# Optimization experiments

Measured on AMD Instinct MI355X. Metric: run time of the kernel, lower is better.

## Reference

```python
import jax, jax.numpy as jnp
import numpy as np

DIM = 1024
NUM_HEADS = 16
HEAD_DIM = DIM // NUM_HEADS
SCALE = HEAD_DIM ** -0.5


def setup_inputs() -> dict:
    key = jax.random.key(0)
    ks = jax.random.split(key, 7)
    b, n = 2, 2048
    x = jax.random.normal(ks[0], (b, n, DIM), dtype=jnp.float32)
    s = DIM ** -0.5
    Wq = jax.random.normal(ks[1], (DIM, DIM), dtype=jnp.float32) * s
    bq = jax.random.normal(ks[2], (DIM,), dtype=jnp.float32) * 0.01
    Wk = jax.random.normal(ks[3], (DIM, DIM), dtype=jnp.float32) * s
    bk = jax.random.normal(ks[4], (DIM,), dtype=jnp.float32) * 0.01
    Wv = jax.random.normal(ks[5], (DIM, DIM), dtype=jnp.float32) * s
    bv = jax.random.normal(ks[6], (DIM,), dtype=jnp.float32) * 0.01
    return {"x": x, "Wq": Wq, "bq": bq, "Wk": Wk, "bk": bk, "Wv": Wv, "bv": bv}


def reference(x, Wq, bq, Wk, bk, Wv, bv):
    b, n, _ = x.shape
    # Linear projections (torch Linear: x @ W.T + b; here W stored as [in, out])
    q = x @ Wq + bq
    k = x @ Wk + bk
    v = x @ Wv + bv
    # split heads: [b, n, h*d] -> [b, h, n, d]
    split = lambda t: t.reshape(b, n, NUM_HEADS, HEAD_DIM).transpose(0, 2, 1, 3)
    q, k, v = split(q), split(k), split(v)
    sim = jnp.einsum('bhid,bhjd->bhij', q, k) * SCALE
    attn = jax.nn.softmax(sim, axis=-1)
    out = jnp.einsum('bhij,bhjd->bhid', attn, v)
    return out.transpose(0, 2, 1, 3).reshape(b, n, DIM)
```

## Files before the change

### kernel.cpp

```cpp
#include <hip/hip_runtime.h>
#include <cstdint>
#include <cstddef>

#define NB    2
#define SEQ   2048
#define DIMC  1024
#define NH    16
#define HDIM  64
#define MROWS (NB*SEQ)
#define NFEAT (3*DIMC)
#define KVBLK 64
#define NT    (SEQ/KVBLK)

typedef _Float16 half8 __attribute__((ext_vector_type(8)));
typedef _Float16 half4 __attribute__((ext_vector_type(4)));
typedef _Float16 half2v __attribute__((ext_vector_type(2)));
typedef __fp16   fp16x2 __attribute__((ext_vector_type(2)));
typedef float    f32x4 __attribute__((ext_vector_type(4)));

typedef const __attribute__((address_space(1))) void* gas_ptr;
typedef __attribute__((address_space(3))) void*       las_ptr;

__device__ __forceinline__ void gload_lds16(const void* g, void* l) {
    __builtin_amdgcn_global_load_lds((gas_ptr)g, (las_ptr)l, 16, 0, 0);
}

__device__ __forceinline__ int swz4(int r) { return (r ^ (r >> 2)) & 3; }

__device__ __forceinline__ float fast_exp2(float x) {
    float r;
    asm("v_exp_f32 %0, %1" : "=v"(r) : "v"(x));
    return r;
}

__device__ __forceinline__ half2v pk_f16(float a, float b) {
    fp16x2 r = __builtin_amdgcn_cvt_pkrtz(a, b);
    return __builtin_bit_cast(half2v, r);
}

__global__ __launch_bounds__(256) void k_convert_x(const float* __restrict__ x,
                                                   _Float16* __restrict__ x16) {
    int i = (blockIdx.x * 256 + threadIdx.x) * 4;
    float4 v = *reinterpret_cast<const float4*>(x + i);
    half4 h = { (_Float16)v.x, (_Float16)v.y, (_Float16)v.z, (_Float16)v.w };
    *reinterpret_cast<half4*>(x16 + i) = h;
}

__global__ __launch_bounds__(256) void k_transpose_w(const float* __restrict__ Wq,
                                                     const float* __restrict__ Wk,
                                                     const float* __restrict__ Wv,
                                                     _Float16* __restrict__ wt) {
    __shared__ float tile[64][65];
    const int bid  = blockIdx.x;
    const int midx = bid >> 8;
    const int t2   = bid & 255;
    const int i0   = (t2 >> 4) * 64;
    const int o0   = (t2 & 15) * 64;
    const float* W = (midx == 0) ? Wq : (midx == 1 ? Wk : Wv);
    const int tid  = threadIdx.x;
    #pragma unroll
    for (int p = 0; p < 4; ++p) {
        int id = p * 256 + tid;
        int r = id >> 4, c4 = (id & 15) * 4;
        float4 v = *reinterpret_cast<const float4*>(W + (size_t)(i0 + r) * DIMC + o0 + c4);
        tile[r][c4 + 0] = v.x; tile[r][c4 + 1] = v.y;
        tile[r][c4 + 2] = v.z; tile[r][c4 + 3] = v.w;
    }
    __syncthreads();
    #pragma unroll
    for (int p = 0; p < 4; ++p) {
        int id = p * 256 + tid;
        int oc = id >> 4, i4 = (id & 15) * 4;
        half4 h = { (_Float16)tile[i4 + 0][oc], (_Float16)tile[i4 + 1][oc],
                    (_Float16)tile[i4 + 2][oc], (_Float16)tile[i4 + 3][oc] };
        *reinterpret_cast<half4*>(wt + (size_t)(midx * DIMC + o0 + oc) * DIMC + i0 + i4) = h;
    }
}

__global__ __launch_bounds__(256) void k_qkv_gemm(
    const _Float16* __restrict__ x16, const _Float16* __restrict__ wt,
    const float* __restrict__ bq, const float* __restrict__ bk, const float* __restrict__ bv,
    _Float16* __restrict__ q16, _Float16* __restrict__ k16, _Float16* __restrict__ vt16)
{
    __shared__ __align__(16) char sraw[49152];
    const int tid = threadIdx.x;
    const int lane = tid & 63;
    const int w = tid >> 6, wm = w >> 1, wn = w & 1;
    const int lr = lane & 15, lg = lane >> 4;
    const int bn = blockIdx.x % (NFEAT / 128);
    const int bm = blockIdx.x / (NFEAT / 128);
    const int m0 = bm * 128, n0 = bn * 128;

    const f32x4 zero4 = {0.f, 0.f, 0.f, 0.f};
    f32x4 acc[4][4];
    #pragma unroll
    for (int i = 0; i < 4; ++i)
        #pragma unroll
        for (int j = 0; j < 4; ++j) acc[i][j] = zero4;

    auto stage = [&](int buf, int kt) {
        const int k0 = kt * 32;
        char* Adst = sraw + buf * 8192;
        char* Bdst = sraw + 24576 + buf * 8192;
        #pragma unroll
        for (int t = 0; t < 2; ++t) {
            int slot = t * 256 + tid;
            int row = slot >> 2, ch = slot & 3;
            int chg = ch ^ swz4(row);
            gload_lds16(x16 + (size_t)(m0 + row) * DIMC + k0 + chg * 8, Adst + slot * 16);
            gload_lds16(wt  + (size_t)(n0 + row) * DIMC + k0 + chg * 8, Bdst + slot * 16);
        }
    };

    stage(0, 0);
    stage(1, 1);
    for (int kt = 0; kt < DIMC / 32; ++kt) {
        if (kt < DIMC / 32 - 1) asm volatile("s_waitcnt vmcnt(4)" ::: "memory");
        else                    asm volatile("s_waitcnt vmcnt(0)" ::: "memory");
        __builtin_amdgcn_s_barrier();
        if (kt + 2 < DIMC / 32) stage((kt + 2) % 3, kt + 2);
        const char* Ab = sraw + (kt % 3) * 8192;
        const char* Bb = sraw + 24576 + (kt % 3) * 8192;
        half8 af[4], bf[4];
        #pragma unroll
        for (int mb = 0; mb < 4; ++mb) {
            int row = wm * 64 + mb * 16 + lr;
            af[mb] = *(const half8*)(Ab + row * 64 + ((lg ^ swz4(row)) << 4));
        }
        #pragma unroll
        for (int nb = 0; nb < 4; ++nb) {
            int col = wn * 64 + nb * 16 + lr;
            bf[nb] = *(const half8*)(Bb + col * 64 + ((lg ^ swz4(col)) << 4));
        }
        #pragma unroll
        for (int mb = 0; mb < 4; ++mb)
            #pragma unroll
            for (int nb = 0; nb < 4; ++nb)
                acc[mb][nb] = __builtin_amdgcn_mfma_f32_16x16x32_f16(af[mb], bf[nb], acc[mb][nb], 0, 0, 0);
    }

    const int sec = n0 >> 10;
    const float* bias = (sec == 0) ? bq : (sec == 1 ? bk : bv);
    const float scl = (sec == 0) ? 0.125f * 1.44269504088896f : 1.0f;
    float bfv[4];
    #pragma unroll
    for (int nb = 0; nb < 4; ++nb)
        bfv[nb] = bias[(n0 & 1023) + wn * 64 + nb * 16 + lr];

    if (sec < 2) {
        _Float16* dst = (sec == 0) ? q16 : k16;
        #pragma unroll
        for (int mb = 0; mb < 4; ++mb)
            #pragma unroll
            for (int i2 = 0; i2 < 4; ++i2) {
                int rg = m0 + wm * 64 + mb * 16 + lg * 4 + i2;
                int bb = rg >> 11, nn = rg & (SEQ - 1);
                #pragma unroll
                for (int nb = 0; nb < 4; ++nb) {
                    int f1 = (n0 & 1023) + wn * 64 + nb * 16 + lr;
                    int hh = f1 >> 6, dd = f1 & 63;
                    dst[((size_t)(bb * NH + hh) * SEQ + nn) * HDIM + dd] =
                        (_Float16)((acc[mb][nb][i2] + bfv[nb]) * scl);
                }
            }
    } else {
        __syncthreads();
        char* lt = sraw;
        #pragma unroll
        for (int mb = 0; mb < 4; ++mb)
            #pragma unroll
            for (int nb = 0; nb < 4; ++nb) {
                int c  = wn * 64 + nb * 16 + lr;
                int r0 = wm * 64 + mb * 16 + lg * 4;
                half4 hv = { (_Float16)(acc[mb][nb][0] + bfv[nb]),
                             (_Float16)(acc[mb][nb][1] + bfv[nb]),
                             (_Float16)(acc[mb][nb][2] + bfv[nb]),
                             (_Float16)(acc[mb][nb][3] + bfv[nb]) };
                *(half4*)(lt + c * 272 + r0 * 2) = hv;
            }
        __syncthreads();
        #pragma unroll
        for (int p = 0; p < 8; ++p) {
            int id = p * 256 + tid;
            int c = id >> 4, r8 = (id & 15) * 8;
            half8 hv = *(const half8*)(lt + c * 272 + r8 * 2);
            int f1 = (n0 & 1023) + c;
            int hh = f1 >> 6, dd = f1 & 63;
            int rg = m0 + r8;
            int bb = rg >> 11, nn = rg & (SEQ - 1);
            *(half8*)(vt16 + ((size_t)(bb * NH + hh) * HDIM + dd) * SEQ + nn) = hv;
        }
    }
}

__global__ __launch_bounds__(512, 4) void k_attn(
    const _Float16* __restrict__ q16, const _Float16* __restrict__ k16,
    const _Float16* __restrict__ vt16, float* __restrict__ out)
{
    __shared__ __align__(16) char lds[81920];
    const int tid = threadIdx.x, lane = tid & 63, w = tid >> 6;
    const int lr = lane & 15, lg = lane >> 4;
    const int sub = w >> 2;
    const int qg  = w & 3;
    const int swz = (blockIdx.x & 7) * 64 + (blockIdx.x >> 3);
    const int bh = swz >> 4;
    const int qt = swz & 15;
    const int qrow0 = qt * 128 + qg * 32;
    const _Float16* qh = q16 + (size_t)bh * SEQ * HDIM;
    const _Float16* kh = k16 + (size_t)bh * SEQ * HDIM;
    const _Float16* vh = vt16 + (size_t)bh * HDIM * SEQ;
    char* pl = lds + 65536 + w * 2048;
    const int rb = lr >> 3;

    const int srow = tid >> 3;
    const int scg  = (tid & 7) ^ (srow & 7);

    auto stageKV = [&](int buf, int t) {
        const int jA = t * KVBLK, jB = (16 + t) * KVBLK;
        gload_lds16(kh + (size_t)(jA + srow) * HDIM + scg * 8,
                    lds + buf * 8192 + tid * 16);
        gload_lds16(kh + (size_t)(jB + srow) * HDIM + scg * 8,
                    lds + 16384 + buf * 8192 + tid * 16);
        gload_lds16(vh + (size_t)srow * SEQ + jA + scg * 8,
                    lds + 32768 + buf * 8192 + tid * 16);
        gload_lds16(vh + (size_t)srow * SEQ + jB + scg * 8,
                    lds + 49152 + buf * 8192 + tid * 16);
    };

    half8 aq[2][2];
    #pragma unroll
    for (int g = 0; g < 2; ++g)
        #pragma unroll
        for (int kc = 0; kc < 2; ++kc)
            aq[g][kc] = *(const half8*)(qh + (size_t)(qrow0 + g * 16 + lr) * HDIM + kc * 32 + lg * 8);

    const f32x4 zero4 = {0.f, 0.f, 0.f, 0.f};
    f32x4 l4[2] = { zero4, zero4 };
    f32x4 oacc[2][4];
    #pragma unroll
    for (int g = 0; g < 2; ++g)
        #pragma unroll
        for (int i = 0; i < 4; ++i) oacc[g][i] = zero4;

    stageKV(0, 0);
    for (int t = 0; t < 16; ++t) {
        __syncthreads();
        if (t + 1 < 16) stageKV((t + 1) & 1, t + 1);
        const char* Kb = lds + sub * 16384 + (t & 1) * 8192;
        const char* Vb = lds + 32768 + sub * 16384 + (t & 1) * 8192;

        f32x4 s0[4], s1[4];
        __builtin_amdgcn_s_setprio(1);
        #pragma unroll
        for (int jb = 0; jb < 4; ++jb) {
            int row = jb * 16 + lr;
            half8 k0 = *(const half8*)(Kb + row * 128 + (((0 + lg) ^ (row & 7)) << 4));
            half8 k1 = *(const half8*)(Kb + row * 128 + (((4 + lg) ^ (row & 7)) << 4));
            f32x4 a0 = __builtin_amdgcn_mfma_f32_16x16x32_f16(k0, aq[0][0], zero4, 0, 0, 0);
            f32x4 a1 = __builtin_amdgcn_mfma_f32_16x16x32_f16(k0, aq[1][0], zero4, 0, 0, 0);
            a0 = __builtin_amdgcn_mfma_f32_16x16x32_f16(k1, aq[0][1], a0, 0, 0, 0);
            a1 = __builtin_amdgcn_mfma_f32_16x16x32_f16(k1, aq[1][1], a1, 0, 0, 0);
            s0[jb] = a0; s1[jb] = a1;
        }
        __builtin_amdgcn_s_setprio(0);

        #pragma unroll
        for (int jb = 0; jb < 4; ++jb) {
            #pragma unroll
            for (int i = 0; i < 4; ++i) s0[jb][i] = fast_exp2(s0[jb][i]);
            l4[0] += s0[jb];
            half2v w0 = pk_f16(s0[jb][0], s0[jb][1]);
            half2v w1 = pk_f16(s0[jb][2], s0[jb][3]);
            half4 pk = { w0.x, w0.y, w1.x, w1.y };
            *(half4*)(pl + lr * 128 + (((jb * 2 + (lg >> 1)) ^ (lr & 7)) << 4)
                      + (((lg & 1) ^ rb) << 3)) = pk;
        }
        half4 pk1[4];
        #pragma unroll
        for (int jb = 0; jb < 4; ++jb) {
            #pragma unroll
            for (int i = 0; i < 4; ++i) s1[jb][i] = fast_exp2(s1[jb][i]);
            l4[1] += s1[jb];
            half2v w0 = pk_f16(s1[jb][0], s1[jb][1]);
            half2v w1 = pk_f16(s1[jb][2], s1[jb][3]);
            pk1[jb] = half4{ w0.x, w0.y, w1.x, w1.y };
        }
        asm volatile("s_waitcnt lgkmcnt(0)" ::: "memory");
        const char* prow = pl + lr * 128;
        half8 ap[2][2];
        {
            half4 l0 = *(const half4*)(prow + (((0 + lg) ^ (lr & 7)) << 4) + (rb << 3));
            half4 h0 = *(const half4*)(prow + (((0 + lg) ^ (lr & 7)) << 4) + ((1 ^ rb) << 3));
            half4 l1 = *(const half4*)(prow + (((4 + lg) ^ (lr & 7)) << 4) + (rb << 3));
            half4 h1 = *(const half4*)(prow + (((4 + lg) ^ (lr & 7)) << 4) + ((1 ^ rb) << 3));
            ap[0][0] = half8{ l0.x, l0.y, l0.z, l0.w, h0.x, h0.y, h0.z, h0.w };
            ap[0][1] = half8{ l1.x, l1.y, l1.z, l1.w, h1.x, h1.y, h1.z, h1.w };
        }
        #pragma unroll
        for (int jb = 0; jb < 4; ++jb)
            *(half4*)(pl + lr * 128 + (((jb * 2 + (lg >> 1)) ^ (lr & 7)) << 4)
                      + (((lg & 1) ^ rb) << 3)) = pk1[jb];
        asm volatile("s_waitcnt lgkmcnt(0)" ::: "memory");
        {
            half4 l0 = *(const half4*)(prow + (((0 + lg) ^ (lr & 7)) << 4) + (rb << 3));
            half4 h0 = *(const half4*)(prow + (((0 + lg) ^ (lr & 7)) << 4) + ((1 ^ rb) << 3));
            half4 l1 = *(const half4*)(prow + (((4 + lg) ^ (lr & 7)) << 4) + (rb << 3));
            half4 h1 = *(const half4*)(prow + (((4 + lg) ^ (lr & 7)) << 4) + ((1 ^ rb) << 3));
            ap[1][0] = half8{ l0.x, l0.y, l0.z, l0.w, h0.x, h0.y, h0.z, h0.w };
            ap[1][1] = half8{ l1.x, l1.y, l1.z, l1.w, h1.x, h1.y, h1.z, h1.w };
        }
        __builtin_amdgcn_s_setprio(1);
        #pragma unroll
        for (int db = 0; db < 4; ++db) {
            int row = db * 16 + lr;
            half8 vf0 = *(const half8*)(Vb + row * 128 + (((0 + lg) ^ (row & 7)) << 4));
            half8 vf1 = *(const half8*)(Vb + row * 128 + (((4 + lg) ^ (row & 7)) << 4));
            oacc[0][db] = __builtin_amdgcn_mfma_f32_16x16x32_f16(ap[0][0], vf0, oacc[0][db], 0, 0, 0);
            oacc[1][db] = __builtin_amdgcn_mfma_f32_16x16x32_f16(ap[1][0], vf0, oacc[1][db], 0, 0, 0);
            oacc[0][db] = __builtin_amdgcn_mfma_f32_16x16x32_f16(ap[0][1], vf1, oacc[0][db], 0, 0, 0);
            oacc[1][db] = __builtin_amdgcn_mfma_f32_16x16x32_f16(ap[1][1], vf1, oacc[1][db], 0, 0, 0);
        }
        __builtin_amdgcn_s_setprio(0);
    }

    __syncthreads();
    char* xch = lds;
    if (sub == 1) {
        char* sl = xch + (qg * 2) * 5120;
        #pragma unroll
        for (int g = 0; g < 2; ++g) {
            #pragma unroll
            for (int db = 0; db < 4; ++db)
                *(f32x4*)(sl + g * 5120 + db * 1024 + lane * 16) = oacc[g][db];
            *(f32x4*)(sl + g * 5120 + 4096 + lane * 16) = l4[g];
        }
    }
    __syncthreads();
    if (sub == 0) {
        char* sl = xch + (qg * 2) * 5120;
        #pragma unroll
        for (int g = 0; g < 2; ++g) {
            #pragma unroll
            for (int db = 0; db < 4; ++db)
                oacc[g][db] += *(const f32x4*)(sl + g * 5120 + db * 1024 + lane * 16);
            l4[g] += *(const f32x4*)(sl + g * 5120 + 4096 + lane * 16);
        }
        const int bb = bh >> 4, hh = bh & 15;
        #pragma unroll
        for (int g = 0; g < 2; ++g) {
            float l_i = (l4[g][0] + l4[g][1]) + (l4[g][2] + l4[g][3]);
            l_i += __shfl_xor(l_i, 16);
            l_i += __shfl_xor(l_i, 32);
            float rlq[4];
            #pragma unroll
            for (int i = 0; i < 4; ++i)
                rlq[i] = 1.0f / __shfl(l_i, lg * 4 + i);
            #pragma unroll
            for (int db = 0; db < 4; ++db)
                #pragma unroll
                for (int i = 0; i < 4; ++i) {
                    int nn = qrow0 + g * 16 + lg * 4 + i;
                    out[((size_t)bb * SEQ + nn) * DIMC + hh * HDIM + db * 16 + lr] =
                        oacc[g][db][i] * rlq[i];
                }
        }
    }
}

extern "C" void kernel_launch(void* const* d_in, const int* in_sizes, int n_in,
                              void* d_out, int out_size, void* d_ws, size_t ws_size,
                              hipStream_t stream)
{
    const float* x  = (const float*)d_in[0];
    const float* Wq = (const float*)d_in[1];
    const float* bq = (const float*)d_in[2];
    const float* Wk = (const float*)d_in[3];
    const float* bk = (const float*)d_in[4];
    const float* Wv = (const float*)d_in[5];
    const float* bv = (const float*)d_in[6];
    float* out = (float*)d_out;

    char* ws = (char*)d_ws;
    _Float16* x16  = (_Float16*)ws;
    _Float16* wt   = (_Float16*)(ws + ((size_t)8  << 20));
    _Float16* q16  = (_Float16*)(ws + ((size_t)14 << 20));
    _Float16* k16  = (_Float16*)(ws + ((size_t)22 << 20));
    _Float16* vt16 = (_Float16*)(ws + ((size_t)30 << 20));

    k_convert_x<<<MROWS * DIMC / 1024, 256, 0, stream>>>(x, x16);
    k_transpose_w<<<3 * 256, 256, 0, stream>>>(Wq, Wk, Wv, wt);
    k_qkv_gemm<<<(MROWS / 128) * (NFEAT / 128), 256, 0, stream>>>(x16, wt, bq, bk, bv,
                                                                  q16, k16, vt16);
    k_attn<<<32 * (SEQ / 128), 512, 0, stream>>>(q16, k16, vt16, out);
}
```

Measured before the change: 92.62 us.

## Feed softmax probabilities directly from registers into 16x16x16 MFMAs for PV

Removes the per-wave LDS round-trip that transposed the exp'd score fragments into the A-operand layout for the PV product. The score accumulator layout is fed directly as the A operand of 16x16x16 f16 MFMAs, and V is read in matching half4 fragments. This cuts LDS writes, reads and waitcnt stalls and shrinks LDS from 80KB to 64KB, which may raise occupancy. In exchange it issues twice as many smaller MFMAs and more, smaller V reads from LDS.

```diff
diff --git a/kernel.cpp b/kernel.cpp
--- a/kernel.cpp
+++ b/kernel.cpp
@@ -197,7 +197,7 @@
     const _Float16* __restrict__ q16, const _Float16* __restrict__ k16,
     const _Float16* __restrict__ vt16, float* __restrict__ out)
 {
-    __shared__ __align__(16) char lds[81920];
+    __shared__ __align__(16) char lds[65536];
     const int tid = threadIdx.x, lane = tid & 63, w = tid >> 6;
     const int lr = lane & 15, lg = lane >> 4;
     const int sub = w >> 2;
@@ -209,8 +209,6 @@
     const _Float16* qh = q16 + (size_t)bh * SEQ * HDIM;
     const _Float16* kh = k16 + (size_t)bh * SEQ * HDIM;
     const _Float16* vh = vt16 + (size_t)bh * HDIM * SEQ;
-    char* pl = lds + 65536 + w * 2048;
-    const int rb = lr >> 3;
 
     const int srow = tid >> 3;
     const int scg  = (tid & 7) ^ (srow & 7);
@@ -264,6 +262,7 @@
         }
         __builtin_amdgcn_s_setprio(0);
 
+        half4 pf0[4], pf1[4];
         #pragma unroll
         for (int jb = 0; jb < 4; ++jb) {
             #pragma unroll
@@ -271,11 +270,8 @@
             l4[0] += s0[jb];
             half2v w0 = pk_f16(s0[jb][0], s0[jb][1]);
             half2v w1 = pk_f16(s0[jb][2], s0[jb][3]);
-            half4 pk = { w0.x, w0.y, w1.x, w1.y };
-            *(half4*)(pl + lr * 128 + (((jb * 2 + (lg >> 1)) ^ (lr & 7)) << 4)
-                      + (((lg & 1) ^ rb) << 3)) = pk;
-        }
-        half4 pk1[4];
+            pf0[jb] = half4{ w0.x, w0.y, w1.x, w1.y };
+        }
         #pragma unroll
         for (int jb = 0; jb < 4; ++jb) {
             #pragma unroll
@@ -283,42 +279,21 @@
             l4[1] += s1[jb];
             half2v w0 = pk_f16(s1[jb][0], s1[jb][1]);
             half2v w1 = pk_f16(s1[jb][2], s1[jb][3]);
-            pk1[jb] = half4{ w0.x, w0.y, w1.x, w1.y };
-        }
-        asm volatile("s_waitcnt lgkmcnt(0)" ::: "memory");
-        const char* prow = pl + lr * 128;
-        half8 ap[2][2];
-        {
-            half4 l0 = *(const half4*)(prow + (((0 + lg) ^ (lr & 7)) << 4) + (rb << 3));
-            half4 h0 = *(const half4*)(prow + (((0 + lg) ^ (lr & 7)) << 4) + ((1 ^ rb) << 3));
-            half4 l1 = *(const half4*)(prow + (((4 + lg) ^ (lr & 7)) << 4) + (rb << 3));
-            half4 h1 = *(const half4*)(prow + (((4 + lg) ^ (lr & 7)) << 4) + ((1 ^ rb) << 3));
-            ap[0][0] = half8{ l0.x, l0.y, l0.z, l0.w, h0.x, h0.y, h0.z, h0.w };
-            ap[0][1] = half8{ l1.x, l1.y, l1.z, l1.w, h1.x, h1.y, h1.z, h1.w };
-        }
-        #pragma unroll
-        for (int jb = 0; jb < 4; ++jb)
-            *(half4*)(pl + lr * 128 + (((jb * 2 + (lg >> 1)) ^ (lr & 7)) << 4)
-                      + (((lg & 1) ^ rb) << 3)) = pk1[jb];
-        asm volatile("s_waitcnt lgkmcnt(0)" ::: "memory");
-        {
-            half4 l0 = *(const half4*)(prow + (((0 + lg) ^ (lr & 7)) << 4) + (rb << 3));
-            half4 h0 = *(const half4*)(prow + (((0 + lg) ^ (lr & 7)) << 4) + ((1 ^ rb) << 3));
-            half4 l1 = *(const half4*)(prow + (((4 + lg) ^ (lr & 7)) << 4) + (rb << 3));
-            half4 h1 = *(const half4*)(prow + (((4 + lg) ^ (lr & 7)) << 4) + ((1 ^ rb) << 3));
-            ap[1][0] = half8{ l0.x, l0.y, l0.z, l0.w, h0.x, h0.y, h0.z, h0.w };
-            ap[1][1] = half8{ l1.x, l1.y, l1.z, l1.w, h1.x, h1.y, h1.z, h1.w };
-        }
+            pf1[jb] = half4{ w0.x, w0.y, w1.x, w1.y };
+        }
+
         __builtin_amdgcn_s_setprio(1);
         #pragma unroll
         for (int db = 0; db < 4; ++db) {
             int row = db * 16 + lr;
-            half8 vf0 = *(const half8*)(Vb + row * 128 + (((0 + lg) ^ (row & 7)) << 4));
-            half8 vf1 = *(const half8*)(Vb + row * 128 + (((4 + lg) ^ (row & 7)) << 4));
-            oacc[0][db] = __builtin_amdgcn_mfma_f32_16x16x32_f16(ap[0][0], vf0, oacc[0][db], 0, 0, 0);
-            oacc[1][db] = __builtin_amdgcn_mfma_f32_16x16x32_f16(ap[1][0], vf0, oacc[1][db], 0, 0, 0);
-            oacc[0][db] = __builtin_amdgcn_mfma_f32_16x16x32_f16(ap[0][1], vf1, oacc[0][db], 0, 0, 0);
-            oacc[1][db] = __builtin_amdgcn_mfma_f32_16x16x32_f16(ap[1][1], vf1, oacc[1][db], 0, 0, 0);
+            const char* vrow = Vb + row * 128;
+            #pragma unroll
+            for (int jb = 0; jb < 4; ++jb) {
+                half4 vf = *(const half4*)(vrow + (((jb * 2 + (lg >> 1)) ^ (row & 7)) << 4)
+                                           + ((lg & 1) << 3));
+                oacc[0][db] = __builtin_amdgcn_mfma_f32_16x16x16f16(pf0[jb], vf, oacc[0][db], 0, 0, 0);
+                oacc[1][db] = __builtin_amdgcn_mfma_f32_16x16x16f16(pf1[jb], vf, oacc[1][db], 0, 0, 0);
+            }
         }
         __builtin_amdgcn_s_setprio(0);
     }
```

Result: slower. 94.55 us (+2.1%).
